# Performance work log

Measured on AMD Instinct MI355X. Metric: run time of the kernel, lower is better.

The kernel has to match this reference:

```python
import jax, jax.numpy as jnp
import numpy as np

ORDER = 2        # order_in1 = order_in2 = order_out = 2
N = 60000        # number of atom pairs (edges)
F = 128          # num_features
B = 32           # num_basis_functions
TRIPLES = [(l1, l2, L) for l1 in range(ORDER + 1) for l2 in range(ORDER + 1)
           for L in range(abs(l1 - l2), min(l1 + l2, ORDER) + 1)]


def setup_inputs():
    key = jax.random.key(0)
    ks = iter(jax.random.split(key, 64))
    inp = {}
    for l in range(ORDER + 1):
        inp[f"x1_{l}"] = jax.random.normal(next(ks), (N, 2 * l + 1, F), jnp.float32)
    for l in range(ORDER + 1):
        inp[f"x2_{l}"] = jax.random.normal(next(ks), (N, 2 * l + 1, F), jnp.float32)
    inp["rbf"] = jax.random.uniform(next(ks), (N, B), jnp.float32)
    for (l1, l2, L) in TRIPLES:
        # fixed Clebsch-Gordan-like constant tensors; real CG tensors are sparse,
        cg = jax.random.normal(next(ks), (2 * l1 + 1, 2 * l2 + 1, 2 * L + 1), jnp.float32)
        mask = jax.random.uniform(next(ks), cg.shape) < 0.3
        inp[f"cg_{l1}_{l2}_{L}"] = jnp.where(mask, cg, 0.0)
        # nn.Linear(B, F, bias=False) weight has shape [F, B]
        inp[f"W_{l1}_{l2}_{L}"] = jax.random.normal(next(ks), (F, B), jnp.float32) / np.sqrt(B)
    return inp


def _pair_mixing(xs1, xs2, rbf, cgs, Ws):
    n = rbf.shape[0]
    f = xs1[0].shape[-1]
    ys = [jnp.zeros((n, 2 * L + 1, f), rbf.dtype) for L in range(ORDER + 1)]
    for i, (l1, l2, L) in enumerate(TRIPLES):
        coeff = rbf @ Ws[i].T                                           # [N, F]
        # fused CG tensor product: sum_{i,j} cg[i,j,k] * x1[n,i,f] * x2[n,j,f]
        tp = jnp.einsum('nif,njf,ijk->nkf', xs1[l1], xs2[l2], cgs[i])   # [N, 2L+1, F]
        ys[L] = ys[L] + coeff[:, None, :] * tp
    return tuple(ys)


def reference(x1_0, x1_1, x1_2, x2_0, x2_1, x2_2, rbf,
              cg_0_0_0, cg_0_1_1, cg_0_2_2, cg_1_0_1, cg_1_1_0, cg_1_1_1, cg_1_1_2,
              cg_1_2_1, cg_1_2_2, cg_2_0_2, cg_2_1_1, cg_2_1_2, cg_2_2_0, cg_2_2_1, cg_2_2_2,
              W_0_0_0, W_0_1_1, W_0_2_2, W_1_0_1, W_1_1_0, W_1_1_1, W_1_1_2,
              W_1_2_1, W_1_2_2, W_2_0_2, W_2_1_1, W_2_1_2, W_2_2_0, W_2_2_1, W_2_2_2):
    loc = locals()
    cgs = [loc[f"cg_{a}_{b}_{c}"] for (a, b, c) in TRIPLES]
    Ws = [loc[f"W_{a}_{b}_{c}"] for (a, b, c) in TRIPLES]
    return _pair_mixing([x1_0, x1_1, x1_2], [x2_0, x2_1, x2_2], rbf, cgs, Ws)
```

## Files before the change

### kernel.cpp

```cpp
#include <hip/hip_runtime.h>


#define NPAIR 60000
#define NB    8
#define Y1OFF (NPAIR * 128)
#define Y2OFF (NPAIR * 128 * 4)
#define WT_BYTES (15 * 128 * 32 * 4)

struct WPtrs { const float* w[15]; };

__global__ void transpose_W_kernel(WPtrs P, float* __restrict__ WT) {
    const int t  = blockIdx.y;
    const int id = blockIdx.x * 256 + threadIdx.x;
    const int f  = id >> 3;
    const int q  = id & 7;
    const float4 v = ((const float4*)(P.w[t] + f * 32))[q];
    ((float4*)WT)[(t * 8 + q) * 128 + f] = v;
}

template<int D1, int D2, int DK>
__device__ __forceinline__ void triple_acc(
    const float* __restrict__ cg,
    const float (&a)[D1][2], const float (&b)[D2][2],
    float cf0, float cf1, float (&y)[DK][2])
{
    float tp[DK][2];
#pragma unroll
    for (int k = 0; k < DK; ++k) { tp[k][0] = 0.f; tp[k][1] = 0.f; }
#pragma unroll
    for (int i = 0; i < D1; ++i) {
#pragma unroll
        for (int j = 0; j < D2; ++j) {
#pragma unroll
            for (int nn = 0; nn < 2; ++nn) {
                const float prod = a[i][nn] * b[j][nn];
#pragma unroll
                for (int k = 0; k < DK; ++k) {
                    tp[k][nn] = fmaf(cg[(i * D2 + j) * DK + k], prod, tp[k][nn]);
                }
            }
        }
    }
#pragma unroll
    for (int k = 0; k < DK; ++k) {
        y[k][0] = fmaf(cf0, tp[k][0], y[k][0]);
        y[k][1] = fmaf(cf1, tp[k][1], y[k][1]);
    }
}

template<bool USE_WT>
__global__ __launch_bounds__(256, 4) void pair_mixing_kernel(
    const float* __restrict__ x1_0, const float* __restrict__ x1_1, const float* __restrict__ x1_2,
    const float* __restrict__ x2_0, const float* __restrict__ x2_1, const float* __restrict__ x2_2,
    const float* __restrict__ rbf,
    const float* __restrict__ cg0,  const float* __restrict__ cg1,  const float* __restrict__ cg2,
    const float* __restrict__ cg3,  const float* __restrict__ cg4,  const float* __restrict__ cg5,
    const float* __restrict__ cg6,  const float* __restrict__ cg7,  const float* __restrict__ cg8,
    const float* __restrict__ cg9,  const float* __restrict__ cg10, const float* __restrict__ cg11,
    const float* __restrict__ cg12, const float* __restrict__ cg13, const float* __restrict__ cg14,
    const float* __restrict__ W0,  const float* __restrict__ W1,  const float* __restrict__ W2,
    const float* __restrict__ W3,  const float* __restrict__ W4,  const float* __restrict__ W5,
    const float* __restrict__ W6,  const float* __restrict__ W7,  const float* __restrict__ W8,
    const float* __restrict__ W9,  const float* __restrict__ W10, const float* __restrict__ W11,
    const float* __restrict__ W12, const float* __restrict__ W13, const float* __restrict__ W14,
    const float* __restrict__ WT,
    float* __restrict__ out)
{
    const int tid = threadIdx.x;
    const int f   = tid & 127;
    const int sub = tid >> 7;
    const int nbt = blockIdx.x * NB + sub * 4;
    const int nbu = __builtin_amdgcn_readfirstlane(nbt);
    const float* rbfp = rbf + ((size_t)nbu << 5);

    const float* Wt[15] = {W0, W1, W2, W3, W4, W5, W6, W7,
                           W8, W9, W10, W11, W12, W13, W14};
    float cf[15][4];
#pragma unroll
    for (int t = 0; t < 15; ++t)
#pragma unroll
        for (int nn = 0; nn < 4; ++nn) cf[t][nn] = 0.f;

#pragma unroll
    for (int q = 0; q < 8; ++q) {
        float rb[4][4];
#pragma unroll
        for (int nn = 0; nn < 4; ++nn)
#pragma unroll
            for (int r = 0; r < 4; ++r)
                rb[nn][r] = rbfp[nn * 32 + q * 4 + r];
#pragma unroll
        for (int t = 0; t < 15; ++t) {
            float4 w;
            if (USE_WT) {
                w = ((const float4*)WT)[(t * 8 + q) * 128 + f];
            } else {
                w = ((const float4*)(Wt[t] + ((size_t)f << 5)))[q];
            }
            const float wv[4] = {w.x, w.y, w.z, w.w};
#pragma unroll
            for (int r = 0; r < 4; ++r)
#pragma unroll
                for (int nn = 0; nn < 4; ++nn)
                    cf[t][nn] = fmaf(rb[nn][r], wv[r], cf[t][nn]);
        }
    }

#pragma unroll
    for (int pass = 0; pass < 2; ++pass) {
        const int nb = nbt + pass * 2;

        float a0[1][2], a1[3][2], a2[5][2];
        float c0[1][2], c1[3][2], c2[5][2];
#pragma unroll
        for (int nn = 0; nn < 2; ++nn) {
            const int n = nb + nn;
            a0[0][nn] = x1_0[n * 128 + f];
#pragma unroll
            for (int i = 0; i < 3; ++i) a1[i][nn] = x1_1[(n * 3 + i) * 128 + f];
#pragma unroll
            for (int i = 0; i < 5; ++i) a2[i][nn] = x1_2[(n * 5 + i) * 128 + f];
            c0[0][nn] = x2_0[n * 128 + f];
#pragma unroll
            for (int j = 0; j < 3; ++j) c1[j][nn] = x2_1[(n * 3 + j) * 128 + f];
#pragma unroll
            for (int j = 0; j < 5; ++j) c2[j][nn] = x2_2[(n * 5 + j) * 128 + f];
        }

        float y0v[1][2], y1v[3][2], y2v[5][2];
#pragma unroll
        for (int k = 0; k < 1; ++k) { y0v[k][0] = 0.f; y0v[k][1] = 0.f; }
#pragma unroll
        for (int k = 0; k < 3; ++k) { y1v[k][0] = 0.f; y1v[k][1] = 0.f; }
#pragma unroll
        for (int k = 0; k < 5; ++k) { y2v[k][0] = 0.f; y2v[k][1] = 0.f; }

        const int p0 = 2 * pass, p1 = 2 * pass + 1;
        triple_acc<1,1,1>(cg0,  a0, c0, cf[0][p0],  cf[0][p1],  y0v);
        triple_acc<1,3,3>(cg1,  a0, c1, cf[1][p0],  cf[1][p1],  y1v);
        triple_acc<1,5,5>(cg2,  a0, c2, cf[2][p0],  cf[2][p1],  y2v);
        triple_acc<3,1,3>(cg3,  a1, c0, cf[3][p0],  cf[3][p1],  y1v);
        triple_acc<3,3,1>(cg4,  a1, c1, cf[4][p0],  cf[4][p1],  y0v);
        triple_acc<3,3,3>(cg5,  a1, c1, cf[5][p0],  cf[5][p1],  y1v);
        triple_acc<3,3,5>(cg6,  a1, c1, cf[6][p0],  cf[6][p1],  y2v);
        triple_acc<3,5,3>(cg7,  a1, c2, cf[7][p0],  cf[7][p1],  y1v);
        triple_acc<3,5,5>(cg8,  a1, c2, cf[8][p0],  cf[8][p1],  y2v);
        triple_acc<5,1,5>(cg9,  a2, c0, cf[9][p0],  cf[9][p1],  y2v);
        triple_acc<5,3,3>(cg10, a2, c1, cf[10][p0], cf[10][p1], y1v);
        triple_acc<5,3,5>(cg11, a2, c1, cf[11][p0], cf[11][p1], y2v);
        triple_acc<5,5,1>(cg12, a2, c2, cf[12][p0], cf[12][p1], y0v);
        triple_acc<5,5,3>(cg13, a2, c2, cf[13][p0], cf[13][p1], y1v);
        triple_acc<5,5,5>(cg14, a2, c2, cf[14][p0], cf[14][p1], y2v);

#pragma unroll
        for (int nn = 0; nn < 2; ++nn) {
            const int n = nb + nn;
            out[n * 128 + f] = y0v[0][nn];
#pragma unroll
            for (int k = 0; k < 3; ++k)
                out[Y1OFF + (n * 3 + k) * 128 + f] = y1v[k][nn];
#pragma unroll
            for (int k = 0; k < 5; ++k)
                out[Y2OFF + (n * 5 + k) * 128 + f] = y2v[k][nn];
        }
    }
}

extern "C" void kernel_launch(void* const* d_in, const int* in_sizes, int n_in,
                              void* d_out, int out_size, void* d_ws, size_t ws_size,
                              hipStream_t stream) {
    const float* x1_0 = (const float*)d_in[0];
    const float* x1_1 = (const float*)d_in[1];
    const float* x1_2 = (const float*)d_in[2];
    const float* x2_0 = (const float*)d_in[3];
    const float* x2_1 = (const float*)d_in[4];
    const float* x2_2 = (const float*)d_in[5];
    const float* rbf  = (const float*)d_in[6];
    const float* cg[15];
    const float* W[15];
    for (int t = 0; t < 15; ++t) {
        cg[t] = (const float*)d_in[7 + 2 * t];
        W[t]  = (const float*)d_in[8 + 2 * t];
    }
    float* out = (float*)d_out;

    const bool use_wt = (d_ws != nullptr) && (ws_size >= (size_t)WT_BYTES);

    dim3 grid(NPAIR / NB);
    dim3 block(256);

    if (use_wt) {
        WPtrs P;
        for (int t = 0; t < 15; ++t) P.w[t] = W[t];
        transpose_W_kernel<<<dim3(4, 15), dim3(256), 0, stream>>>(P, (float*)d_ws);
        pair_mixing_kernel<true><<<grid, block, 0, stream>>>(
            x1_0, x1_1, x1_2, x2_0, x2_1, x2_2, rbf,
            cg[0], cg[1], cg[2], cg[3], cg[4], cg[5], cg[6], cg[7],
            cg[8], cg[9], cg[10], cg[11], cg[12], cg[13], cg[14],
            W[0], W[1], W[2], W[3], W[4], W[5], W[6], W[7],
            W[8], W[9], W[10], W[11], W[12], W[13], W[14],
            (const float*)d_ws, out);
    } else {
        pair_mixing_kernel<false><<<grid, block, 0, stream>>>(
            x1_0, x1_1, x1_2, x2_0, x2_1, x2_2, rbf,
            cg[0], cg[1], cg[2], cg[3], cg[4], cg[5], cg[6], cg[7],
            cg[8], cg[9], cg[10], cg[11], cg[12], cg[13], cg[14],
            W[0], W[1], W[2], W[3], W[4], W[5], W[6], W[7],
            W[8], W[9], W[10], W[11], W[12], W[13], W[14],
            nullptr, out);
    }
}
```

Measured before the change: 1.124 ms.

## Remap threads to two features each and use packed FP32 FMA

Each thread now handles two adjacent features for two pairs, where before it handled one feature for four pairs. The math is written with float2 vector types so the compiler can emit packed FMA (v_pk_fma_f32) and 64-bit loads and stores. The W pre-pack kernel interleaves even and odd feature rows to match the new mapping. This aims to halve VALU instruction count and widen memory accesses, at the cost of more scalar CG broadcasts per packed op and a changed register footprint.

```diff
diff --git a/kernel.cpp b/kernel.cpp
--- a/kernel.cpp
+++ b/kernel.cpp
@@ -7,45 +7,66 @@
 #define Y2OFF (NPAIR * 128 * 4)
 #define WT_BYTES (15 * 128 * 32 * 4)
 
+typedef float f32x2 __attribute__((ext_vector_type(2)));
+typedef float f32x4 __attribute__((ext_vector_type(4)));
+
+__device__ __forceinline__ f32x2 pkfma(f32x2 a, f32x2 b, f32x2 c) {
+#if defined(__has_builtin)
+#if __has_builtin(__builtin_elementwise_fma)
+    return __builtin_elementwise_fma(a, b, c);
+#else
+    f32x2 r; r.x = fmaf(a.x, b.x, c.x); r.y = fmaf(a.y, b.y, c.y); return r;
+#endif
+#else
+    f32x2 r; r.x = fmaf(a.x, b.x, c.x); r.y = fmaf(a.y, b.y, c.y); return r;
+#endif
+}
+__device__ __forceinline__ f32x2 bc(float s) { f32x2 r; r.x = s; r.y = s; return r; }
+__device__ __forceinline__ f32x2 mk2(float a, float b) { f32x2 r; r.x = a; r.y = b; return r; }
+__device__ __forceinline__ f32x2 ld2(const float* p) { return *(const f32x2*)p; }
+__device__ __forceinline__ void st2(float* p, f32x2 v) { *(f32x2*)p = v; }
+
 struct WPtrs { const float* w[15]; };
 
-__global__ void transpose_W_kernel(WPtrs P, float* __restrict__ WT) {
-    const int t  = blockIdx.y;
+__global__ void pack_W_kernel(WPtrs P, float* __restrict__ WT) {
     const int id = blockIdx.x * 256 + threadIdx.x;
-    const int f  = id >> 3;
-    const int q  = id & 7;
-    const float4 v = ((const float4*)(P.w[t] + f * 32))[q];
-    ((float4*)WT)[(t * 8 + q) * 128 + f] = v;
+    if (id >= 15 * 8 * 64) return;
+    const int t = id >> 9;
+    const int q = (id >> 6) & 7;
+    const int l = id & 63;
+    const float* w = P.w[t];
+    const f32x4 e = *(const f32x4*)(w + (size_t)(2 * l) * 32 + 4 * q);
+    const f32x4 o = *(const f32x4*)(w + (size_t)(2 * l + 1) * 32 + 4 * q);
+    f32x4* dst = (f32x4*)WT + (size_t)id * 2;
+    f32x4 d0; d0.x = e.x; d0.y = o.x; d0.z = e.y; d0.w = o.y;
+    f32x4 d1; d1.x = e.z; d1.y = o.z; d1.z = e.w; d1.w = o.w;
+    dst[0] = d0;
+    dst[1] = d1;
 }
 
 template<int D1, int D2, int DK>
 __device__ __forceinline__ void triple_acc(
     const float* __restrict__ cg,
-    const float (&a)[D1][2], const float (&b)[D2][2],
-    float cf0, float cf1, float (&y)[DK][2])
+    const f32x2 (&a)[D1], const f32x2 (&b)[D2],
+    f32x2 cf, f32x2 (&y)[DK])
 {
-    float tp[DK][2];
-#pragma unroll
-    for (int k = 0; k < DK; ++k) { tp[k][0] = 0.f; tp[k][1] = 0.f; }
+    f32x2 tp[DK];
+#pragma unroll
+    for (int k = 0; k < DK; ++k) { tp[k].x = 0.f; tp[k].y = 0.f; }
 #pragma unroll
     for (int i = 0; i < D1; ++i) {
 #pragma unroll
         for (int j = 0; j < D2; ++j) {
-#pragma unroll
-            for (int nn = 0; nn < 2; ++nn) {
-                const float prod = a[i][nn] * b[j][nn];
-#pragma unroll
-                for (int k = 0; k < DK; ++k) {
-                    tp[k][nn] = fmaf(cg[(i * D2 + j) * DK + k], prod, tp[k][nn]);
-                }
+            const f32x2 prod = a[i] * b[j];
+#pragma unroll
+            for (int k = 0; k < DK; ++k) {
+                tp[k] = pkfma(bc(cg[(i * D2 + j) * DK + k]), prod, tp[k]);
             }
         }
     }
 #pragma unroll
-    for (int k = 0; k < DK; ++k) {
-        y[k][0] = fmaf(cf0, tp[k][0], y[k][0]);
-        y[k][1] = fmaf(cf1, tp[k][1], y[k][1]);
-    }
+    for (int k = 0; k < DK; ++k)
+        y[k] = pkfma(cf, tp[k], y[k]);
 }
 
 template<bool USE_WT>
@@ -67,102 +88,100 @@
     float* __restrict__ out)
 {
     const int tid = threadIdx.x;
-    const int f   = tid & 127;
-    const int sub = tid >> 7;
-    const int nbt = blockIdx.x * NB + sub * 4;
-    const int nbu = __builtin_amdgcn_readfirstlane(nbt);
+    const int l   = tid & 63;
+    const int wv  = tid >> 6;
+    const int f0  = l << 1;
+    const int nb  = blockIdx.x * NB + wv * 2;
+    const int nbu = __builtin_amdgcn_readfirstlane(nb);
     const float* rbfp = rbf + ((size_t)nbu << 5);
 
     const float* Wt[15] = {W0, W1, W2, W3, W4, W5, W6, W7,
                            W8, W9, W10, W11, W12, W13, W14};
-    float cf[15][4];
-#pragma unroll
-    for (int t = 0; t < 15; ++t)
-#pragma unroll
-        for (int nn = 0; nn < 4; ++nn) cf[t][nn] = 0.f;
+
+    f32x2 cf[15][2];
+#pragma unroll
+    for (int t = 0; t < 15; ++t) { cf[t][0] = bc(0.f); cf[t][1] = bc(0.f); }
 
 #pragma unroll
     for (int q = 0; q < 8; ++q) {
-        float rb[4][4];
-#pragma unroll
-        for (int nn = 0; nn < 4; ++nn)
+        float rb[2][4];
+#pragma unroll
+        for (int nn = 0; nn < 2; ++nn)
 #pragma unroll
             for (int r = 0; r < 4; ++r)
                 rb[nn][r] = rbfp[nn * 32 + q * 4 + r];
 #pragma unroll
         for (int t = 0; t < 15; ++t) {
-            float4 w;
+            f32x2 wb[4];
             if (USE_WT) {
-                w = ((const float4*)WT)[(t * 8 + q) * 128 + f];
+                const f32x4* wp = (const f32x4*)WT + (size_t)((t * 8 + q) * 64 + l) * 2;
+                const f32x4 wA = wp[0];
+                const f32x4 wB = wp[1];
+                wb[0] = mk2(wA.x, wA.y); wb[1] = mk2(wA.z, wA.w);
+                wb[2] = mk2(wB.x, wB.y); wb[3] = mk2(wB.z, wB.w);
             } else {
-                w = ((const float4*)(Wt[t] + ((size_t)f << 5)))[q];
+                const f32x4 e = *(const f32x4*)(Wt[t] + (size_t)f0 * 32 + 4 * q);
+                const f32x4 o = *(const f32x4*)(Wt[t] + (size_t)(f0 + 1) * 32 + 4 * q);
+                wb[0] = mk2(e.x, o.x);
+                wb[1] = mk2(e.y, o.y);
+                wb[2] = mk2(e.z, o.z);
+                wb[3] = mk2(e.w, o.w);
             }
-            const float wv[4] = {w.x, w.y, w.z, w.w};
-#pragma unroll
-            for (int r = 0; r < 4; ++r)
-#pragma unroll
-                for (int nn = 0; nn < 4; ++nn)
-                    cf[t][nn] = fmaf(rb[nn][r], wv[r], cf[t][nn]);
+#pragma unroll
+            for (int r = 0; r < 4; ++r) {
+                cf[t][0] = pkfma(bc(rb[0][r]), wb[r], cf[t][0]);
+                cf[t][1] = pkfma(bc(rb[1][r]), wb[r], cf[t][1]);
+            }
         }
     }
 
 #pragma unroll
     for (int pass = 0; pass < 2; ++pass) {
-        const int nb = nbt + pass * 2;
-
-        float a0[1][2], a1[3][2], a2[5][2];
-        float c0[1][2], c1[3][2], c2[5][2];
-#pragma unroll
-        for (int nn = 0; nn < 2; ++nn) {
-            const int n = nb + nn;
-            a0[0][nn] = x1_0[n * 128 + f];
-#pragma unroll
-            for (int i = 0; i < 3; ++i) a1[i][nn] = x1_1[(n * 3 + i) * 128 + f];
-#pragma unroll
-            for (int i = 0; i < 5; ++i) a2[i][nn] = x1_2[(n * 5 + i) * 128 + f];
-            c0[0][nn] = x2_0[n * 128 + f];
-#pragma unroll
-            for (int j = 0; j < 3; ++j) c1[j][nn] = x2_1[(n * 3 + j) * 128 + f];
-#pragma unroll
-            for (int j = 0; j < 5; ++j) c2[j][nn] = x2_2[(n * 5 + j) * 128 + f];
-        }
-
-        float y0v[1][2], y1v[3][2], y2v[5][2];
-#pragma unroll
-        for (int k = 0; k < 1; ++k) { y0v[k][0] = 0.f; y0v[k][1] = 0.f; }
-#pragma unroll
-        for (int k = 0; k < 3; ++k) { y1v[k][0] = 0.f; y1v[k][1] = 0.f; }
-#pragma unroll
-        for (int k = 0; k < 5; ++k) { y2v[k][0] = 0.f; y2v[k][1] = 0.f; }
-
-        const int p0 = 2 * pass, p1 = 2 * pass + 1;
-        triple_acc<1,1,1>(cg0,  a0, c0, cf[0][p0],  cf[0][p1],  y0v);
-        triple_acc<1,3,3>(cg1,  a0, c1, cf[1][p0],  cf[1][p1],  y1v);
-        triple_acc<1,5,5>(cg2,  a0, c2, cf[2][p0],  cf[2][p1],  y2v);
-        triple_acc<3,1,3>(cg3,  a1, c0, cf[3][p0],  cf[3][p1],  y1v);
-        triple_acc<3,3,1>(cg4,  a1, c1, cf[4][p0],  cf[4][p1],  y0v);
-        triple_acc<3,3,3>(cg5,  a1, c1, cf[5][p0],  cf[5][p1],  y1v);
-        triple_acc<3,3,5>(cg6,  a1, c1, cf[6][p0],  cf[6][p1],  y2v);
-        triple_acc<3,5,3>(cg7,  a1, c2, cf[7][p0],  cf[7][p1],  y1v);
-        triple_acc<3,5,5>(cg8,  a1, c2, cf[8][p0],  cf[8][p1],  y2v);
-        triple_acc<5,1,5>(cg9,  a2, c0, cf[9][p0],  cf[9][p1],  y2v);
-        triple_acc<5,3,3>(cg10, a2, c1, cf[10][p0], cf[10][p1], y1v);
-        triple_acc<5,3,5>(cg11, a2, c1, cf[11][p0], cf[11][p1], y2v);
-        triple_acc<5,5,1>(cg12, a2, c2, cf[12][p0], cf[12][p1], y0v);
-        triple_acc<5,5,3>(cg13, a2, c2, cf[13][p0], cf[13][p1], y1v);
-        triple_acc<5,5,5>(cg14, a2, c2, cf[14][p0], cf[14][p1], y2v);
-
-#pragma unroll
-        for (int nn = 0; nn < 2; ++nn) {
-            const int n = nb + nn;
-            out[n * 128 + f] = y0v[0][nn];
-#pragma unroll
-            for (int k = 0; k < 3; ++k)
-                out[Y1OFF + (n * 3 + k) * 128 + f] = y1v[k][nn];
-#pragma unroll
-            for (int k = 0; k < 5; ++k)
-                out[Y2OFF + (n * 5 + k) * 128 + f] = y2v[k][nn];
-        }
+        const int n = nb + pass;
+
+        f32x2 a0[1], a1[3], a2[5], c0[1], c1[3], c2[5];
+        a0[0] = ld2(x1_0 + (size_t)n * 128 + f0);
+#pragma unroll
+        for (int i = 0; i < 3; ++i) a1[i] = ld2(x1_1 + (size_t)(n * 3 + i) * 128 + f0);
+#pragma unroll
+        for (int i = 0; i < 5; ++i) a2[i] = ld2(x1_2 + (size_t)(n * 5 + i) * 128 + f0);
+        c0[0] = ld2(x2_0 + (size_t)n * 128 + f0);
+#pragma unroll
+        for (int j = 0; j < 3; ++j) c1[j] = ld2(x2_1 + (size_t)(n * 3 + j) * 128 + f0);
+#pragma unroll
+        for (int j = 0; j < 5; ++j) c2[j] = ld2(x2_2 + (size_t)(n * 5 + j) * 128 + f0);
+
+        f32x2 y0v[1], y1v[3], y2v[5];
+#pragma unroll
+        for (int k = 0; k < 1; ++k) y0v[k] = bc(0.f);
+#pragma unroll
+        for (int k = 0; k < 3; ++k) y1v[k] = bc(0.f);
+#pragma unroll
+        for (int k = 0; k < 5; ++k) y2v[k] = bc(0.f);
+
+        triple_acc<1,1,1>(cg0,  a0, c0, cf[0][pass],  y0v);
+        triple_acc<1,3,3>(cg1,  a0, c1, cf[1][pass],  y1v);
+        triple_acc<1,5,5>(cg2,  a0, c2, cf[2][pass],  y2v);
+        triple_acc<3,1,3>(cg3,  a1, c0, cf[3][pass],  y1v);
+        triple_acc<3,3,1>(cg4,  a1, c1, cf[4][pass],  y0v);
+        triple_acc<3,3,3>(cg5,  a1, c1, cf[5][pass],  y1v);
+        triple_acc<3,3,5>(cg6,  a1, c1, cf[6][pass],  y2v);
+        triple_acc<3,5,3>(cg7,  a1, c2, cf[7][pass],  y1v);
+        triple_acc<3,5,5>(cg8,  a1, c2, cf[8][pass],  y2v);
+        triple_acc<5,1,5>(cg9,  a2, c0, cf[9][pass],  y2v);
+        triple_acc<5,3,3>(cg10, a2, c1, cf[10][pass], y1v);
+        triple_acc<5,3,5>(cg11, a2, c1, cf[11][pass], y2v);
+        triple_acc<5,5,1>(cg12, a2, c2, cf[12][pass], y0v);
+        triple_acc<5,5,3>(cg13, a2, c2, cf[13][pass], y1v);
+        triple_acc<5,5,5>(cg14, a2, c2, cf[14][pass], y2v);
+
+        st2(out + (size_t)n * 128 + f0, y0v[0]);
+#pragma unroll
+        for (int k = 0; k < 3; ++k)
+            st2(out + (size_t)Y1OFF + (size_t)(n * 3 + k) * 128 + f0, y1v[k]);
+#pragma unroll
+        for (int k = 0; k < 5; ++k)
+            st2(out + (size_t)Y2OFF + (size_t)(n * 5 + k) * 128 + f0, y2v[k]);
     }
 }
 
@@ -192,7 +211,7 @@
     if (use_wt) {
         WPtrs P;
         for (int t = 0; t < 15; ++t) P.w[t] = W[t];
-        transpose_W_kernel<<<dim3(4, 15), dim3(256), 0, stream>>>(P, (float*)d_ws);
+        pack_W_kernel<<<dim3(30), dim3(256), 0, stream>>>(P, (float*)d_ws);
         pair_mixing_kernel<true><<<grid, block, 0, stream>>>(
             x1_0, x1_1, x1_2, x2_0, x2_1, x2_2, rbf,
             cg[0], cg[1], cg[2], cg[3], cg[4], cg[5], cg[6], cg[7],
```

After: 1.301 ms. +15.8%, slower.
